# Optimization experiments

Measured on AMD Instinct MI355X. Metric: run time of the kernel, lower is better.

The kernel has to match this reference:

```python
import jax, jax.numpy as jnp
import numpy as np

N_NODES = 50000
N_EDGES = 800000
D_IN = 128
D_OUT = 64


def setup_inputs() -> dict:
    key = jax.random.key(0)
    k1, k2, k3, k4, k5 = jax.random.split(key, 5)
    x = jax.random.normal(k1, (N_NODES, D_IN), dtype=jnp.float32)
    edge_src = jax.random.randint(k2, (N_EDGES,), 0, N_NODES, dtype=jnp.int32)
    edge_dst = jax.random.randint(k3, (N_EDGES,), 0, N_NODES, dtype=jnp.int32)
    edge_vals = jax.random.uniform(k4, (N_EDGES,), dtype=jnp.float32)
    # xavier_normal init for weight, zeros for bias (matches torch init)
    std = float(np.sqrt(2.0 / (D_IN + D_OUT)))
    W = jax.random.normal(k5, (D_IN, D_OUT), dtype=jnp.float32) * std
    b = jnp.zeros((D_OUT,), dtype=jnp.float32)
    return {"x": x, "edge_src": edge_src, "edge_dst": edge_dst,
            "edge_vals": edge_vals, "W": W, "b": b}


def reference(x, edge_src, edge_dst, edge_vals, W, b):
    # support = x @ W  : dense feature transform [N, D_OUT]
    support = jnp.dot(x, W)
    # sparse adj @ support via gather + weighted segment-sum over edges
    # adj[dst, src] = edge_vals  ->  out[dst] = sum_e vals[e] * support[src[e]]
    msgs = support[edge_src] * edge_vals[:, None]  # [E, D_OUT]
    out = jax.ops.segment_sum(msgs, edge_dst, num_segments=N_NODES)
    out = out + b
    return jax.nn.relu(out)
```

## Files before the change

kernel.cpp:

```cpp
#include <hip/hip_runtime.h>
#include <hip/hip_fp16.h>

#define N_NODES 50000
#define N_EDGES_MAX 800000
#define D_IN    128
#define D_OUT   64

#define BW      32
#define BSHIFT  5
#define NBKT    ((N_NODES + BW - 1) / BW)
#define BPAD    2048
#define PCHUNK  2048
#define HCHUNK  2048
#define ACH     2048

#define NPB 16

__global__ __launch_bounds__(256) void gemm_xw(
    const float* __restrict__ x, const float* __restrict__ W,
    __half* __restrict__ support, int* __restrict__ gcnt,
    int* __restrict__ done) {
  const int tid = threadIdx.x;
  if (blockIdx.x == 0) {
#pragma unroll
    for (int i = 0; i < BPAD / 256; ++i) gcnt[tid + i * 256] = 0;
    if (tid == 0) *done = 0;
  }

  __shared__ float Wlds[D_IN][D_OUT];
  __shared__ float xlds[NPB][D_IN];
  const int node0 = blockIdx.x * NPB;

  const float4* W4 = (const float4*)W;
  float4* Wl4 = (float4*)Wlds;
#pragma unroll
  for (int i = 0; i < (D_IN * D_OUT / 4) / 256; ++i)
    Wl4[tid + i * 256] = W4[tid + i * 256];

  const float4* x4 = (const float4*)(x + (size_t)node0 * D_IN);
  float4* xl4 = (float4*)xlds;
#pragma unroll
  for (int i = 0; i < (NPB * D_IN / 4) / 256; ++i)
    xl4[tid + i * 256] = x4[tid + i * 256];

  __syncthreads();

  const int f = tid & 63;
  const int g = tid >> 6;
  float acc0 = 0.f, acc1 = 0.f, acc2 = 0.f, acc3 = 0.f;

#pragma unroll
  for (int k = 0; k < D_IN; k += 4) {
    const float w0 = Wlds[k + 0][f];
    const float w1 = Wlds[k + 1][f];
    const float w2 = Wlds[k + 2][f];
    const float w3 = Wlds[k + 3][f];
    const float4 xa = *(const float4*)&xlds[g * 4 + 0][k];
    const float4 xb = *(const float4*)&xlds[g * 4 + 1][k];
    const float4 xc = *(const float4*)&xlds[g * 4 + 2][k];
    const float4 xd = *(const float4*)&xlds[g * 4 + 3][k];
    acc0 += xa.x * w0 + xa.y * w1 + xa.z * w2 + xa.w * w3;
    acc1 += xb.x * w0 + xb.y * w1 + xb.z * w2 + xb.w * w3;
    acc2 += xc.x * w0 + xc.y * w1 + xc.z * w2 + xc.w * w3;
    acc3 += xd.x * w0 + xd.y * w1 + xd.z * w2 + xd.w * w3;
  }

  const int nbase = node0 + g * 4;
  support[(size_t)(nbase + 0) * D_OUT + f] = __float2half(acc0);
  support[(size_t)(nbase + 1) * D_OUT + f] = __float2half(acc1);
  support[(size_t)(nbase + 2) * D_OUT + f] = __float2half(acc2);
  support[(size_t)(nbase + 3) * D_OUT + f] = __float2half(acc3);
}

__global__ __launch_bounds__(256) void hist_scan(
    const int* __restrict__ edst, int* __restrict__ gcnt,
    int* __restrict__ goff, int* __restrict__ gcur,
    int* __restrict__ done, int n_edges) {
  __shared__ int lh[BPAD];
  __shared__ int wsum[4], wpre[4];
  __shared__ int lastflag;
  const int t = threadIdx.x;
  for (int b = t; b < BPAD; b += 256) lh[b] = 0;
  __syncthreads();
  const int e0 = blockIdx.x * HCHUNK;
  const int e1 = min(e0 + HCHUNK, n_edges);
  for (int i = e0 + t; i < e1; i += 256)
    atomicAdd(&lh[edst[i] >> BSHIFT], 1);
  __syncthreads();
  for (int b = t; b < BPAD; b += 256) {
    const int c = lh[b];
    if (c) atomicAdd(&gcnt[b], c);
  }
  __threadfence();
  if (t == 0) lastflag = (atomicAdd(done, 1) == (int)gridDim.x - 1) ? 1 : 0;
  __syncthreads();
  if (!lastflag) return;
  __threadfence();

  const int lane = t & 63, w = t >> 6;
  int c[8];
  int s = 0;
#pragma unroll
  for (int k = 0; k < 8; ++k) {
    c[k] = atomicAdd(&gcnt[8 * t + k], 0);
    s += c[k];
  }
  int incl = s;
#pragma unroll
  for (int off = 1; off < 64; off <<= 1) {
    const int u = __shfl_up(incl, off);
    if (lane >= off) incl += u;
  }
  if (lane == 63) wsum[w] = incl;
  __syncthreads();
  if (t == 0) {
    int run = 0;
#pragma unroll
    for (int i = 0; i < 4; ++i) { wpre[i] = run; run += wsum[i]; }
  }
  __syncthreads();
  int ex = wpre[w] + incl - s;
#pragma unroll
  for (int k = 0; k < 8; ++k) {
    goff[8 * t + k] = ex;
    gcur[8 * t + k] = ex;
    ex += c[k];
  }
}

__global__ __launch_bounds__(512) void partition(
    const int* __restrict__ esrc, const int* __restrict__ edst,
    const float* __restrict__ eval, int* __restrict__ gcur,
    int2* __restrict__ svp, int n_edges) {
  __shared__ int lh[BPAD], lscan[BPAD], lcur[BPAD], lbase[BPAD];
  __shared__ int wsum[8], wpre[8];
  __shared__ int2 stage[PCHUNK];
  const int t = threadIdx.x;
  const int lane = t & 63, w = t >> 6;
  const int e0 = blockIdx.x * PCHUNK;
  const int e1 = min(e0 + PCHUNK, n_edges);

  lh[t] = 0; lh[t + 512] = 0; lh[t + 1024] = 0; lh[t + 1536] = 0;
  __syncthreads();

  int  rs[4], rd[4];
  float rv[4];
#pragma unroll
  for (int k = 0; k < 4; ++k) {
    const int i = e0 + t + k * 512;
    if (i < e1) {
      rs[k] = esrc[i]; rd[k] = edst[i]; rv[k] = eval[i];
      atomicAdd(&lh[rd[k] >> BSHIFT], 1);
    } else {
      rs[k] = -1; rd[k] = 0; rv[k] = 0.f;
    }
  }
  __syncthreads();

  const int a0 = lh[4 * t], a1 = lh[4 * t + 1];
  const int a2 = lh[4 * t + 2], a3 = lh[4 * t + 3];
  const int s = a0 + a1 + a2 + a3;
  int incl = s;
#pragma unroll
  for (int off = 1; off < 64; off <<= 1) {
    const int u = __shfl_up(incl, off);
    if (lane >= off) incl += u;
  }
  if (lane == 63) wsum[w] = incl;
  __syncthreads();
  if (t == 0) {
    int run = 0;
#pragma unroll
    for (int i = 0; i < 8; ++i) { wpre[i] = run; run += wsum[i]; }
  }
  __syncthreads();
  const int ex = wpre[w] + incl - s;
  lscan[4 * t]     = ex;
  lscan[4 * t + 1] = ex + a0;
  lscan[4 * t + 2] = ex + a0 + a1;
  lscan[4 * t + 3] = ex + a0 + a1 + a2;
  lcur[4 * t]      = ex;
  lcur[4 * t + 1]  = ex + a0;
  lcur[4 * t + 2]  = ex + a0 + a1;
  lcur[4 * t + 3]  = ex + a0 + a1 + a2;
  if (a0) lbase[4 * t]     = atomicAdd(&gcur[4 * t],     a0);
  if (a1) lbase[4 * t + 1] = atomicAdd(&gcur[4 * t + 1], a1);
  if (a2) lbase[4 * t + 2] = atomicAdd(&gcur[4 * t + 2], a2);
  if (a3) lbase[4 * t + 3] = atomicAdd(&gcur[4 * t + 3], a3);
  __syncthreads();

#pragma unroll
  for (int k = 0; k < 4; ++k) {
    if (rs[k] >= 0) {
      const int b = rd[k] >> BSHIFT;
      const int r = atomicAdd(&lcur[b], 1);
      stage[r] = make_int2(rs[k] | ((rd[k] & (BW - 1)) << 16) | (b << 21),
                           __float_as_int(rv[k]));
    }
  }
  __syncthreads();

  const int kn = e1 - e0;
  if (kn == PCHUNK) {
    const int2 E0 = stage[t];
    const int2 E1 = stage[t + 512];
    const int2 E2 = stage[t + 1024];
    const int2 E3 = stage[t + 1536];
    const int b0 = (int)((unsigned)E0.x >> 21);
    const int b1 = (int)((unsigned)E1.x >> 21);
    const int b2i = (int)((unsigned)E2.x >> 21);
    const int b3 = (int)((unsigned)E3.x >> 21);
    svp[lbase[b0] + (t         - lscan[b0])] = make_int2(E0.x & 0x1FFFFF, E0.y);
    svp[lbase[b1] + (t + 512  - lscan[b1])] = make_int2(E1.x & 0x1FFFFF, E1.y);
    svp[lbase[b2i] + (t + 1024 - lscan[b2i])] = make_int2(E2.x & 0x1FFFFF, E2.y);
    svp[lbase[b3] + (t + 1536 - lscan[b3])] = make_int2(E3.x & 0x1FFFFF, E3.y);
  } else {
    for (int p = t; p < kn; p += 512) {
      const int2 e = stage[p];
      const int b = (int)((unsigned)e.x >> 21);
      svp[lbase[b] + (p - lscan[b])] = make_int2(e.x & 0x1FFFFF, e.y);
    }
  }
}

__global__ __launch_bounds__(256) void aggregate_bucket(
    const __half* __restrict__ support, const int* __restrict__ goff,
    const int2* __restrict__ svp, const float* __restrict__ bias,
    float* __restrict__ out) {
  __shared__ int2 sorted[ACH];
  __shared__ int h[BW];
  __shared__ int ro[BW + 1];
  __shared__ int cur[BW];
  const int t = threadIdx.x;
  const int f = t & 63;
  const int wid = t >> 6;
  const int bkt = blockIdx.x;
  const int beg = goff[bkt];
  const int end = goff[bkt + 1];

  float acc[8];
#pragma unroll
  for (int k = 0; k < 8; ++k) acc[k] = 0.f;

  for (int cbeg = beg; cbeg < end; cbeg += ACH) {
    const int cn = min(ACH, end - cbeg);
    if (t < BW) h[t] = 0;
    __syncthreads();

    int2 m[8];
#pragma unroll
    for (int k = 0; k < 8; ++k) {
      const int i = t + k * 256;
      if (i < cn) {
        m[k] = svp[cbeg + i];
        atomicAdd(&h[(m[k].x >> 16) & (BW - 1)], 1);
      } else {
        m[k] = make_int2(-1, 0);
      }
    }
    __syncthreads();

    if (wid == 0) {
      const int c = (f < BW) ? h[f] : 0;
      int v = c;
#pragma unroll
      for (int off = 1; off < 64; off <<= 1) {
        const int u = __shfl_up(v, off);
        if (f >= off) v += u;
      }
      if (f < BW) { ro[f] = v - c; cur[f] = v - c; }
      if (f == BW - 1) ro[BW] = cn;
    }
    __syncthreads();

#pragma unroll
    for (int k = 0; k < 8; ++k) {
      if (m[k].x >= 0) {
        const int r = atomicAdd(&cur[(m[k].x >> 16) & (BW - 1)], 1);
        sorted[r] = m[k];
      }
    }
    __syncthreads();

#pragma unroll
    for (int k = 0; k < 8; ++k) {
      const int row = wid * 8 + k;
      int j = ro[row];
      const int re = ro[row + 1];
      for (; j + 8 <= re; j += 8) {
        int2 e[8];
#pragma unroll
        for (int u = 0; u < 8; ++u) e[u] = sorted[j + u];
        float s[8];
#pragma unroll
        for (int u = 0; u < 8; ++u)
          s[u] = __half2float(support[(size_t)(e[u].x & 0xFFFF) * D_OUT + f]);
#pragma unroll
        for (int u = 0; u < 8; ++u)
          acc[k] = fmaf(s[u], __int_as_float(e[u].y), acc[k]);
      }
      for (; j < re; ++j) {
        const int2 e = sorted[j];
        acc[k] = fmaf(__half2float(support[(size_t)(e.x & 0xFFFF) * D_OUT + f]),
                      __int_as_float(e.y), acc[k]);
      }
    }
    __syncthreads();
  }

  const float bf = bias[f];
  const int nbase = bkt * BW;
#pragma unroll
  for (int k = 0; k < 8; ++k) {
    const int node = nbase + wid * 8 + k;
    if (node < N_NODES)
      out[(size_t)node * D_OUT + f] = fmaxf(acc[k] + bf, 0.f);
  }
}

#define EPG 8
__global__ __launch_bounds__(256) void scatter_edges(
    const __half* __restrict__ support, const int* __restrict__ esrc,
    const int* __restrict__ edst, const float* __restrict__ eval,
    float* __restrict__ out, int n_edges) {
  const int tid = threadIdx.x;
  const int f = tid & 63;
  const int grp = blockIdx.x * 4 + (tid >> 6);
  const int e0 = grp * EPG;
  int s[EPG], d[EPG];
  float v[EPG];
#pragma unroll
  for (int i = 0; i < EPG; ++i) {
    const int e = e0 + i;
    if (e < n_edges) { s[i] = esrc[e]; d[i] = edst[e]; v[i] = eval[e]; }
    else             { s[i] = 0; d[i] = 0; v[i] = 0.f; }
  }
  float m[EPG];
#pragma unroll
  for (int i = 0; i < EPG; ++i)
    m[i] = __half2float(support[(size_t)s[i] * D_OUT + f]) * v[i];
#pragma unroll
  for (int i = 0; i < EPG; ++i)
    if (e0 + i < n_edges) atomicAdd(&out[(size_t)d[i] * D_OUT + f], m[i]);
}

__global__ __launch_bounds__(256) void bias_relu(
    float* __restrict__ out, const float* __restrict__ b) {
  const int i = blockIdx.x * 256 + threadIdx.x;
  float4* o4 = (float4*)out;
  float4 v = o4[i];
  const int fb = (i * 4) & 63;
  const float4 bb = *(const float4*)&b[fb];
  v.x = fmaxf(v.x + bb.x, 0.f);
  v.y = fmaxf(v.y + bb.y, 0.f);
  v.z = fmaxf(v.z + bb.z, 0.f);
  v.w = fmaxf(v.w + bb.w, 0.f);
  o4[i] = v;
}

extern "C" void kernel_launch(void* const* d_in, const int* in_sizes, int n_in,
                              void* d_out, int out_size, void* d_ws, size_t ws_size,
                              hipStream_t stream) {
  const float* x    = (const float*)d_in[0];
  const int*   esrc = (const int*)  d_in[1];
  const int*   edst = (const int*)  d_in[2];
  const float* eval = (const float*)d_in[3];
  const float* W    = (const float*)d_in[4];
  const float* b    = (const float*)d_in[5];
  float* out = (float*)d_out;
  const int n_edges = in_sizes[1];

  size_t off = 0;
  auto alloc = [&](size_t bytes) {
    size_t o = off;
    off = (off + bytes + 255) & ~(size_t)255;
    return o;
  };
  char* ws = (char*)d_ws;
  const size_t sup_o  = alloc((size_t)N_NODES * D_OUT * sizeof(__half));
  const size_t cnt_o  = alloc((size_t)BPAD * sizeof(int));
  const size_t offs_o = alloc((size_t)BPAD * sizeof(int));
  const size_t cur_o  = alloc((size_t)BPAD * sizeof(int));
  const size_t done_o = alloc(256);
  const size_t svp_o  = alloc((size_t)N_EDGES_MAX * sizeof(int2));
  const size_t req = off;

  __half* support = (__half*)(ws + sup_o);
  int* gcnt = (int*)(ws + cnt_o);
  int* done = (int*)(ws + done_o);

  if (ws_size >= req && n_edges <= N_EDGES_MAX) {
    int*  goff = (int*) (ws + offs_o);
    int*  gcur = (int*) (ws + cur_o);
    int2* svp  = (int2*)(ws + svp_o);

    gemm_xw<<<N_NODES / NPB, 256, 0, stream>>>(x, W, support, gcnt, done);
    hist_scan<<<(n_edges + HCHUNK - 1) / HCHUNK, 256, 0, stream>>>(
        edst, gcnt, goff, gcur, done, n_edges);
    partition<<<(n_edges + PCHUNK - 1) / PCHUNK, 512, 0, stream>>>(
        esrc, edst, eval, gcur, svp, n_edges);
    aggregate_bucket<<<NBKT, 256, 0, stream>>>(support, goff, svp, b, out);
  } else {
    gemm_xw<<<N_NODES / NPB, 256, 0, stream>>>(x, W, support, gcnt, done);
    hipMemsetAsync(d_out, 0, (size_t)N_NODES * D_OUT * sizeof(float), stream);
    const int groups = (n_edges + EPG - 1) / EPG;
    scatter_edges<<<(groups + 3) / 4, 256, 0, stream>>>(support, esrc, edst,
                                                        eval, out, n_edges);
    bias_relu<<<N_NODES * D_OUT / 4 / 256, 256, 0, stream>>>(out, b);
  }
}
```

Baseline: 200.0 us.

## Fuse GEMM and edge histogram into one launch with block-range dispatch

```diff
diff --git a/kernel.cpp b/kernel.cpp
--- a/kernel.cpp
+++ b/kernel.cpp
@@ -15,86 +15,81 @@
 #define ACH     2048
 
 #define NPB 16
-
-__global__ __launch_bounds__(256) void gemm_xw(
+#define GB  (N_NODES / NPB)
+
+__global__ __launch_bounds__(256) void gemm_hist(
     const float* __restrict__ x, const float* __restrict__ W,
-    __half* __restrict__ support, int* __restrict__ gcnt,
-    int* __restrict__ done) {
-  const int tid = threadIdx.x;
-  if (blockIdx.x == 0) {
-#pragma unroll
-    for (int i = 0; i < BPAD / 256; ++i) gcnt[tid + i * 256] = 0;
-    if (tid == 0) *done = 0;
-  }
-
-  __shared__ float Wlds[D_IN][D_OUT];
-  __shared__ float xlds[NPB][D_IN];
-  const int node0 = blockIdx.x * NPB;
-
-  const float4* W4 = (const float4*)W;
-  float4* Wl4 = (float4*)Wlds;
-#pragma unroll
-  for (int i = 0; i < (D_IN * D_OUT / 4) / 256; ++i)
-    Wl4[tid + i * 256] = W4[tid + i * 256];
-
-  const float4* x4 = (const float4*)(x + (size_t)node0 * D_IN);
-  float4* xl4 = (float4*)xlds;
-#pragma unroll
-  for (int i = 0; i < (NPB * D_IN / 4) / 256; ++i)
-    xl4[tid + i * 256] = x4[tid + i * 256];
-
-  __syncthreads();
-
-  const int f = tid & 63;
-  const int g = tid >> 6;
-  float acc0 = 0.f, acc1 = 0.f, acc2 = 0.f, acc3 = 0.f;
-
-#pragma unroll
-  for (int k = 0; k < D_IN; k += 4) {
-    const float w0 = Wlds[k + 0][f];
-    const float w1 = Wlds[k + 1][f];
-    const float w2 = Wlds[k + 2][f];
-    const float w3 = Wlds[k + 3][f];
-    const float4 xa = *(const float4*)&xlds[g * 4 + 0][k];
-    const float4 xb = *(const float4*)&xlds[g * 4 + 1][k];
-    const float4 xc = *(const float4*)&xlds[g * 4 + 2][k];
-    const float4 xd = *(const float4*)&xlds[g * 4 + 3][k];
-    acc0 += xa.x * w0 + xa.y * w1 + xa.z * w2 + xa.w * w3;
-    acc1 += xb.x * w0 + xb.y * w1 + xb.z * w2 + xb.w * w3;
-    acc2 += xc.x * w0 + xc.y * w1 + xc.z * w2 + xc.w * w3;
-    acc3 += xd.x * w0 + xd.y * w1 + xd.z * w2 + xd.w * w3;
-  }
-
-  const int nbase = node0 + g * 4;
-  support[(size_t)(nbase + 0) * D_OUT + f] = __float2half(acc0);
-  support[(size_t)(nbase + 1) * D_OUT + f] = __float2half(acc1);
-  support[(size_t)(nbase + 2) * D_OUT + f] = __float2half(acc2);
-  support[(size_t)(nbase + 3) * D_OUT + f] = __float2half(acc3);
-}
-
-__global__ __launch_bounds__(256) void hist_scan(
-    const int* __restrict__ edst, int* __restrict__ gcnt,
-    int* __restrict__ goff, int* __restrict__ gcur,
+    __half* __restrict__ support, const int* __restrict__ edst,
+    int* __restrict__ gcnt, int* __restrict__ goff, int* __restrict__ gcur,
     int* __restrict__ done, int n_edges) {
-  __shared__ int lh[BPAD];
-  __shared__ int wsum[4], wpre[4];
-  __shared__ int lastflag;
+  __shared__ union {
+    struct { float Wl[D_IN][D_OUT]; float xl[NPB][D_IN]; } g;
+    struct { int lh[BPAD]; int wsum[4]; int wpre[4]; int lastflag; } h;
+  } sm;
   const int t = threadIdx.x;
-  for (int b = t; b < BPAD; b += 256) lh[b] = 0;
-  __syncthreads();
-  const int e0 = blockIdx.x * HCHUNK;
+
+  if (blockIdx.x < GB) {
+    const int node0 = blockIdx.x * NPB;
+
+    const float4* W4 = (const float4*)W;
+    float4* Wl4 = (float4*)sm.g.Wl;
+#pragma unroll
+    for (int i = 0; i < (D_IN * D_OUT / 4) / 256; ++i)
+      Wl4[t + i * 256] = W4[t + i * 256];
+
+    const float4* x4 = (const float4*)(x + (size_t)node0 * D_IN);
+    float4* xl4 = (float4*)sm.g.xl;
+#pragma unroll
+    for (int i = 0; i < (NPB * D_IN / 4) / 256; ++i)
+      xl4[t + i * 256] = x4[t + i * 256];
+
+    __syncthreads();
+
+    const int f = t & 63;
+    const int g = t >> 6;
+    float acc0 = 0.f, acc1 = 0.f, acc2 = 0.f, acc3 = 0.f;
+
+#pragma unroll
+    for (int k = 0; k < D_IN; k += 4) {
+      const float w0 = sm.g.Wl[k + 0][f];
+      const float w1 = sm.g.Wl[k + 1][f];
+      const float w2 = sm.g.Wl[k + 2][f];
+      const float w3 = sm.g.Wl[k + 3][f];
+      const float4 xa = *(const float4*)&sm.g.xl[g * 4 + 0][k];
+      const float4 xb = *(const float4*)&sm.g.xl[g * 4 + 1][k];
+      const float4 xc = *(const float4*)&sm.g.xl[g * 4 + 2][k];
+      const float4 xd = *(const float4*)&sm.g.xl[g * 4 + 3][k];
+      acc0 += xa.x * w0 + xa.y * w1 + xa.z * w2 + xa.w * w3;
+      acc1 += xb.x * w0 + xb.y * w1 + xb.z * w2 + xb.w * w3;
+      acc2 += xc.x * w0 + xc.y * w1 + xc.z * w2 + xc.w * w3;
+      acc3 += xd.x * w0 + xd.y * w1 + xd.z * w2 + xd.w * w3;
+    }
+
+    const int nbase = node0 + g * 4;
+    support[(size_t)(nbase + 0) * D_OUT + f] = __float2half(acc0);
+    support[(size_t)(nbase + 1) * D_OUT + f] = __float2half(acc1);
+    support[(size_t)(nbase + 2) * D_OUT + f] = __float2half(acc2);
+    support[(size_t)(nbase + 3) * D_OUT + f] = __float2half(acc3);
+    return;
+  }
+
+  const int hb  = blockIdx.x - GB;
+  const int nhb = (int)gridDim.x - GB;
+  for (int b = t; b < BPAD; b += 256) sm.h.lh[b] = 0;
+  __syncthreads();
+  const int e0 = hb * HCHUNK;
   const int e1 = min(e0 + HCHUNK, n_edges);
   for (int i = e0 + t; i < e1; i += 256)
-    atomicAdd(&lh[edst[i] >> BSHIFT], 1);
+    atomicAdd(&sm.h.lh[edst[i] >> BSHIFT], 1);
   __syncthreads();
   for (int b = t; b < BPAD; b += 256) {
-    const int c = lh[b];
+    const int c = sm.h.lh[b];
     if (c) atomicAdd(&gcnt[b], c);
   }
   __threadfence();
-  if (t == 0) lastflag = (atomicAdd(done, 1) == (int)gridDim.x - 1) ? 1 : 0;
-  __syncthreads();
-  if (!lastflag) return;
+  if (t == 0) sm.h.lastflag = (atomicAdd(done, 1) == nhb - 1) ? 1 : 0;
+  __syncthreads();
+  if (!sm.h.lastflag) return;
   __threadfence();
 
   const int lane = t & 63, w = t >> 6;
@@ -111,15 +106,15 @@
     const int u = __shfl_up(incl, off);
     if (lane >= off) incl += u;
   }
-  if (lane == 63) wsum[w] = incl;
+  if (lane == 63) sm.h.wsum[w] = incl;
   __syncthreads();
   if (t == 0) {
     int run = 0;
 #pragma unroll
-    for (int i = 0; i < 4; ++i) { wpre[i] = run; run += wsum[i]; }
-  }
-  __syncthreads();
-  int ex = wpre[w] + incl - s;
+    for (int i = 0; i < 4; ++i) { sm.h.wpre[i] = run; run += sm.h.wsum[i]; }
+  }
+  __syncthreads();
+  int ex = sm.h.wpre[w] + incl - s;
 #pragma unroll
   for (int k = 0; k < 8; ++k) {
     goff[8 * t + k] = ex;
@@ -379,29 +374,33 @@
   char* ws = (char*)d_ws;
   const size_t sup_o  = alloc((size_t)N_NODES * D_OUT * sizeof(__half));
   const size_t cnt_o  = alloc((size_t)BPAD * sizeof(int));
+  const size_t done_o = alloc(256);
   const size_t offs_o = alloc((size_t)BPAD * sizeof(int));
   const size_t cur_o  = alloc((size_t)BPAD * sizeof(int));
-  const size_t done_o = alloc(256);
   const size_t svp_o  = alloc((size_t)N_EDGES_MAX * sizeof(int2));
   const size_t req = off;
 
   __half* support = (__half*)(ws + sup_o);
-  int* gcnt = (int*)(ws + cnt_o);
-  int* done = (int*)(ws + done_o);
 
   if (ws_size >= req && n_edges <= N_EDGES_MAX) {
+    int*  gcnt = (int*) (ws + cnt_o);
+    int*  done = (int*) (ws + done_o);
     int*  goff = (int*) (ws + offs_o);
     int*  gcur = (int*) (ws + cur_o);
     int2* svp  = (int2*)(ws + svp_o);
 
-    gemm_xw<<<N_NODES / NPB, 256, 0, stream>>>(x, W, support, gcnt, done);
-    hist_scan<<<(n_edges + HCHUNK - 1) / HCHUNK, 256, 0, stream>>>(
-        edst, gcnt, goff, gcur, done, n_edges);
+    hipMemsetAsync(gcnt, 0, (size_t)BPAD * sizeof(int) + 256, stream);
+
+    const int nhb = (n_edges + HCHUNK - 1) / HCHUNK;
+    gemm_hist<<<GB + nhb, 256, 0, stream>>>(x, W, support, edst,
+                                            gcnt, goff, gcur, done, n_edges);
     partition<<<(n_edges + PCHUNK - 1) / PCHUNK, 512, 0, stream>>>(
         esrc, edst, eval, gcur, svp, n_edges);
     aggregate_bucket<<<NBKT, 256, 0, stream>>>(support, goff, svp, b, out);
   } else {
-    gemm_xw<<<N_NODES / NPB, 256, 0, stream>>>(x, W, support, gcnt, done);
+    gemm_hist<<<GB, 256, 0, stream>>>(x, W, support, edst,
+                                      (int*)d_ws, (int*)d_ws, (int*)d_ws,
+                                      (int*)d_ws, n_edges);
     hipMemsetAsync(d_out, 0, (size_t)N_NODES * D_OUT * sizeof(float), stream);
     const int groups = (n_edges + EPG - 1) / EPG;
     scatter_edges<<<(groups + 3) / 4, 256, 0, stream>>>(support, esrc, edst,
```

New measurement: 206.3 us. +3.2%, slower.
